# Kernel optimization log

Measured on AMD Instinct MI355X. Metric: run time of the kernel, lower is better.

## Reference

```python
import jax, jax.numpy as jnp
import numpy as np

TAU = 5.0
ENTROPY_REG = 0.0  # entropy branch disabled (matches init kwargs)
NEG_INF = -1.0e9
NORM_EPS = 1e-12   # F.normalize eps
COS_EPS = 1e-8     # F.cosine_similarity eps


def _l2norm(x):
    n = jnp.sqrt(jnp.sum(x * x, axis=-1, keepdims=True))
    return x / jnp.maximum(n, NORM_EPS)


def setup_inputs() -> dict:
    key = jax.random.key(0)
    k1, k2, k3 = jax.random.split(key, 3)
    B, T, D = 8, 2048, 512
    pred_tokens = jax.random.normal(k1, (B, T, D), dtype=jnp.float32)
    text_tokens = jax.random.normal(k2, (B, T, D), dtype=jnp.float32)
    text_pad_mask = jax.random.randint(k3, (B, T), 0, 2).astype(jnp.bool_)  # True = PAD
    return {"pred_tokens": pred_tokens, "text_tokens": text_tokens, "text_pad_mask": text_pad_mask}


def reference(pred_tokens, text_tokens, text_pad_mask):
    B, Tp, D = pred_tokens.shape
    Tt = text_tokens.shape[1]
    T = min(Tp, Tt)
    P = _l2norm(pred_tokens[:, :T, :])            # [B,T,D]
    E = _l2norm(text_tokens[:, :T, :])            # [B,T,D]
    valid = ~text_pad_mask[:, :T]                 # [B,T] True = valid column

    S = jnp.einsum('btd,bsd->bts', P, E)          # [B,T,T]
    S = jnp.where(valid[:, None, :], S, NEG_INF)
    A = jax.nn.softmax(S * TAU, axis=-1)          # [B,T,T]
    E_hat = jnp.einsum('bts,bsd->btd', A, E)      # [B,T,D]

    # cosine similarity with eps-clamped norms (F.cosine_similarity semantics)
    dot = jnp.sum(P * E_hat, axis=-1)             # [B,T]
    pn = jnp.maximum(jnp.sqrt(jnp.sum(P * P, axis=-1)), COS_EPS)
    en = jnp.maximum(jnp.sqrt(jnp.sum(E_hat * E_hat, axis=-1)), COS_EPS)
    cos = dot / (pn * en)                         # [B,T]

    # row_has_valid: per-batch 'any valid column', broadcast over rows
    row_valid = jnp.broadcast_to(jnp.any(valid, axis=-1, keepdims=True), cos.shape)
    w = row_valid.astype(cos.dtype)
    cnt = jnp.sum(w)
    loss_sel = jnp.sum(w * (1.0 - cos)) / jnp.maximum(cnt, 1.0)
    loss = jnp.where(cnt > 0, loss_sel, jnp.zeros((), cos.dtype))
    tas = jnp.where(cnt > 0, 1.0 - jax.lax.stop_gradient(loss), loss)
    return (loss, tas)
```

## Files before the change

kernel.cpp:

```cpp
#include <hip/hip_runtime.h>
#include <cstdint>

typedef float f32x4 __attribute__((ext_vector_type(4)));
typedef long longx2 __attribute__((ext_vector_type(2)));
typedef unsigned char u8;
typedef unsigned short u16;
typedef unsigned int u32;
typedef unsigned long long u64;

#define B_N 8
#define T_N 2048
#define D_N 512
#define TAU 5.0f
#define NROW (B_N * T_N)
#define K1E 7.213475204444817f
#define K2E 1.4426950408889634f

#define WAITV(n) asm volatile("s_waitcnt vmcnt(" #n ")" ::: "memory")
#define BAR      __builtin_amdgcn_s_barrier()

__device__ __forceinline__ void gload_lds16(const u8* g, u8* l) {
  __builtin_amdgcn_global_load_lds(
      (const __attribute__((address_space(1))) u32*)g,
      (__attribute__((address_space(3))) u32*)l, 16, 0, 0);
}

__device__ __forceinline__ u32 pk4_fp8(float a, float b, float c, float d) {
  int w = __builtin_amdgcn_cvt_pk_fp8_f32(a, b, 0, 0);
  w = __builtin_amdgcn_cvt_pk_fp8_f32(c, d, w, 1);
  return (u32)w;
}

__device__ __forceinline__ u16 f2bf16(float x) {
  u32 u = __builtin_bit_cast(u32, x);
  u32 r = u + 0x7fffu + ((u >> 16) & 1u);
  return (u16)(r >> 16);
}
__device__ __forceinline__ float bf2f(u16 v) {
  u32 u = ((u32)v) << 16;
  return __builtin_bit_cast(float, u);
}

__global__ void kprep(const float* __restrict__ text,
                      u8* __restrict__ EF, u8* __restrict__ ET) {
  __shared__ u8 tile[32][528];
  int b = blockIdx.y, t = blockIdx.x;
  int tr = threadIdx.x;
  int row = tr >> 3, seg = tr & 7;
  const float* src = text + ((size_t)b * T_N + t * 32 + row) * D_N + seg * 64;
  float4 v[16];
  float ss = 0.f;
#pragma unroll
  for (int j = 0; j < 16; ++j) {
    v[j] = *(const float4*)(src + j * 4);
    ss += v[j].x*v[j].x + v[j].y*v[j].y + v[j].z*v[j].z + v[j].w*v[j].w;
  }
  ss += __shfl_xor(ss, 1); ss += __shfl_xor(ss, 2); ss += __shfl_xor(ss, 4);
  float inv = 1.f / fmaxf(sqrtf(ss), 1e-12f);
  u32 w[16];
#pragma unroll
  for (int j = 0; j < 16; ++j)
    w[j] = pk4_fp8(v[j].x*inv, v[j].y*inv, v[j].z*inv, v[j].w*inv);
  uint4* ldst = (uint4*)&tile[row][seg * 64];
#pragma unroll
  for (int j = 0; j < 4; ++j)
    ldst[j] = make_uint4(w[4*j], w[4*j+1], w[4*j+2], w[4*j+3]);
  __syncthreads();
  size_t tbase = ((size_t)(b * 64 + t)) << 14;
  {
    int j = tr >> 5, tok = tr & 31;
    u32 acc[16];
#pragma unroll
    for (int g2 = 0; g2 < 4; ++g2)
#pragma unroll
      for (int h = 0; h < 2; ++h) {
        uint2 vv = *(const uint2*)&tile[tok][j*64 + h*32 + g2*8];
        acc[g2*4 + h*2] = vv.x; acc[g2*4 + h*2 + 1] = vv.y;
      }
    uint4* dst = (uint4*)(EF + tbase + tr * 64);
#pragma unroll
    for (int q = 0; q < 4; ++q)
      dst[q] = make_uint4(acc[4*q], acc[4*q+1], acc[4*q+2], acc[4*q+3]);
  }
  {
    int m = tr >> 4, g2 = (tr >> 2) & 3, c0 = (tr & 3) * 4;
    u32 acc[16];
#pragma unroll
    for (int ci = 0; ci < 4; ++ci)
#pragma unroll
      for (int h = 0; h < 2; ++h) {
        int c = c0 + ci, n = 2*m + h;
        u32 lo = 0, hi = 0;
#pragma unroll
        for (int e = 0; e < 4; ++e) lo |= (u32)tile[g2*4 + e][n*16 + c] << (8*e);
#pragma unroll
        for (int e = 0; e < 4; ++e) hi |= (u32)tile[16 + g2*4 + e][n*16 + c] << (8*e);
        acc[ci*4 + h*2] = lo; acc[ci*4 + h*2 + 1] = hi;
      }
    uint4* dst = (uint4*)(ET + tbase + tr * 64);
#pragma unroll
    for (int q = 0; q < 4; ++q)
      dst[q] = make_uint4(acc[4*q], acc[4*q+1], acc[4*q+2], acc[4*q+3]);
  }
}

__launch_bounds__(512, 2)
__global__ void kflash(const float* __restrict__ pred,
                       const u8* __restrict__ EF, const u8* __restrict__ ET,
                       const int* __restrict__ mask,
                       u16* __restrict__ Opart, float* __restrict__ Lpart,
                       float* __restrict__ Dpart) {
  int b = blockIdx.x & 7;
  int rem = blockIdx.x >> 3;
  int rb = rem & 15, h = rem >> 4;
  int wid = threadIdx.x >> 6, lane = threadIdx.x & 63;
  int g = lane >> 4, c = lane & 15;
  int row0 = rb * 128 + wid * 16;
  int t0 = h * 32;

  __shared__ u64 mbits[32];
  __shared__ __align__(16) u8 els[2][16384];
  __shared__ __align__(16) u8 etls[2][16384];

  const u8* EFb = EF + (((size_t)(b * 64)) << 14) + (lane << 4);
  const u8* ETb = ET + (((size_t)(b * 64)) << 14) + (lane << 4);

  auto stageE = [&](int buf, int t) {
    size_t tb = ((size_t)t) << 14;
#pragma unroll
    for (int j = 0; j < 2; ++j) {
      int ch = wid * 2 + j;
      gload_lds16(EFb + tb + (ch << 10), &els[buf][ch << 10]);
    }
  };
  auto stageET = [&](int buf, int t) {
    size_t tb = ((size_t)t) << 14;
#pragma unroll
    for (int j = 0; j < 2; ++j) {
      int ch = wid * 2 + j;
      gload_lds16(ETb + tb + (ch << 10), &etls[buf][ch << 10]);
    }
  };

  for (int chunk = wid; chunk < 32; chunk += 8) {
    int col = chunk * 64 + lane;
    u64 bal = __ballot(mask[b * T_N + col] == 0);
    if (lane == 0) mbits[chunk] = bal;
  }

  stageE(0, t0); stageET(0, t0); stageE(1, t0 + 1);

  long pf[16];
  {
    int prow = row0 + c;
    const float* pr = pred + ((size_t)(b * T_N) + prow) * D_N;
    float ss = 0.f;
#pragma unroll
    for (int kk = 0; kk < 16; ++kk) {
      float4 v0 = *(const float4*)(pr + kk * 32 + g * 8);
      float4 v1 = *(const float4*)(pr + kk * 32 + g * 8 + 4);
      ss += v0.x*v0.x + v0.y*v0.y + v0.z*v0.z + v0.w*v0.w
          + v1.x*v1.x + v1.y*v1.y + v1.z*v1.z + v1.w*v1.w;
    }
    ss += __shfl_xor(ss, 16);
    ss += __shfl_xor(ss, 32);
    float inv = 1.f / fmaxf(sqrtf(ss), 1e-12f);
#pragma unroll
    for (int kk = 0; kk < 16; ++kk) {
      float4 v0 = *(const float4*)(pr + kk * 32 + g * 8);
      float4 v1 = *(const float4*)(pr + kk * 32 + g * 8 + 4);
      u32 lo = pk4_fp8(v0.x*inv, v0.y*inv, v0.z*inv, v0.w*inv);
      u32 hi = pk4_fp8(v1.x*inv, v1.y*inv, v1.z*inv, v1.w*inv);
      pf[kk] = (long)(((u64)hi << 32) | lo);
    }
  }

  __syncthreads();

  f32x4 zero = {0.f, 0.f, 0.f, 0.f};
  f32x4 eh[32];
#pragma unroll
  for (int n = 0; n < 32; ++n) eh[n] = zero;
  float lsum = 0.f, dsum = 0.f;

  const int sb_off = c * 64 + g * 16;
  const int pv_off = g * 256 + c * 16;

#pragma unroll 1
  for (int tt = 0; tt < 32; ++tt) {
    int cur = tt & 1;
    if (tt < 31) { WAITV(2); } else { WAITV(0); }
    BAR;

    if (tt < 31) stageET(cur ^ 1, t0 + tt + 1);
    const u8* el = &els[cur][0];
    f32x4 ta0 = zero, tb0 = zero, ta1 = zero, tb1 = zero;
    __builtin_amdgcn_s_setprio(1);
#pragma unroll
    for (int j = 0; j < 4; ++j) {
      longx2 b0 = *(const longx2*)(el + j * 2048 + sb_off);
      longx2 b1 = *(const longx2*)(el + j * 2048 + 1024 + sb_off);
      ta0 = __builtin_amdgcn_mfma_f32_16x16x32_fp8_fp8(b0[0], pf[2*j],   ta0, 0, 0, 0);
      tb0 = __builtin_amdgcn_mfma_f32_16x16x32_fp8_fp8(b0[1], pf[2*j+1], tb0, 0, 0, 0);
      ta1 = __builtin_amdgcn_mfma_f32_16x16x32_fp8_fp8(b1[0], pf[2*j],   ta1, 0, 0, 0);
      tb1 = __builtin_amdgcn_mfma_f32_16x16x32_fp8_fp8(b1[1], pf[2*j+1], tb1, 0, 0, 0);
    }
    __builtin_amdgcn_s_setprio(0);
    BAR;

    __builtin_amdgcn_s_setprio(1);
#pragma unroll
    for (int j = 4; j < 8; ++j) {
      longx2 b0 = *(const longx2*)(el + j * 2048 + sb_off);
      longx2 b1 = *(const longx2*)(el + j * 2048 + 1024 + sb_off);
      ta0 = __builtin_amdgcn_mfma_f32_16x16x32_fp8_fp8(b0[0], pf[2*j],   ta0, 0, 0, 0);
      tb0 = __builtin_amdgcn_mfma_f32_16x16x32_fp8_fp8(b0[1], pf[2*j+1], tb0, 0, 0, 0);
      ta1 = __builtin_amdgcn_mfma_f32_16x16x32_fp8_fp8(b1[0], pf[2*j],   ta1, 0, 0, 0);
      tb1 = __builtin_amdgcn_mfma_f32_16x16x32_fp8_fp8(b1[1], pf[2*j+1], tb1, 0, 0, 0);
    }
    __builtin_amdgcn_s_setprio(0);
    f32x4 st0 = ta0 + tb0, st1 = ta1 + tb1;
    BAR;

    if (tt < 30) stageE(cur, t0 + tt + 2);
    int c0 = (t0 + tt) * 32;
    u64 mw = mbits[c0 >> 6];
    u32 sh0 = (c0 & 63) + g * 4;
    u32 bits0 = (u32)(mw >> sh0) & 0xf;
    u32 bits1 = (u32)(mw >> (sh0 + 16)) & 0xf;
    float p0[4], p1[4];
#pragma unroll
    for (int r = 0; r < 4; ++r) {
      p0[r] = (bits0 >> r) & 1 ? __builtin_exp2f(fmaf(K1E, st0[r], -K2E)) : 0.f;
      p1[r] = (bits1 >> r) & 1 ? __builtin_exp2f(fmaf(K1E, st1[r], -K2E)) : 0.f;
      lsum += p0[r] + p1[r];
      dsum += p0[r] * st0[r] + p1[r] * st1[r];
    }
    u32 lo = pk4_fp8(p0[0], p0[1], p0[2], p0[3]);
    u32 hi = pk4_fp8(p1[0], p1[1], p1[2], p1[3]);
    long af = (long)(((u64)hi << 32) | lo);

    const u8* et = &etls[cur][0];
    __builtin_amdgcn_s_setprio(1);
#pragma unroll
    for (int m = 0; m < 8; ++m) {
      longx2 bv = *(const longx2*)(et + m * 1024 + pv_off);
      eh[2*m]   = __builtin_amdgcn_mfma_f32_16x16x32_fp8_fp8(af, bv[0], eh[2*m],   0, 0, 0);
      eh[2*m+1] = __builtin_amdgcn_mfma_f32_16x16x32_fp8_fp8(af, bv[1], eh[2*m+1], 0, 0, 0);
    }
    __builtin_amdgcn_s_setprio(0);
    BAR;

    __builtin_amdgcn_s_setprio(1);
#pragma unroll
    for (int m = 8; m < 16; ++m) {
      longx2 bv = *(const longx2*)(et + m * 1024 + pv_off);
      eh[2*m]   = __builtin_amdgcn_mfma_f32_16x16x32_fp8_fp8(af, bv[0], eh[2*m],   0, 0, 0);
      eh[2*m+1] = __builtin_amdgcn_mfma_f32_16x16x32_fp8_fp8(af, bv[1], eh[2*m+1], 0, 0, 0);
    }
    __builtin_amdgcn_s_setprio(0);
  }

  lsum += __shfl_xor(lsum, 16);
  lsum += __shfl_xor(lsum, 32);
  dsum += __shfl_xor(dsum, 16);
  dsum += __shfl_xor(dsum, 32);
  u16* OP = Opart + (size_t)h * ((size_t)NROW * D_N);
#pragma unroll
  for (int r = 0; r < 4; ++r) {
    int brow = b * T_N + row0 + g * 4 + r;
    u16* orow = OP + (size_t)brow * D_N + c;
#pragma unroll
    for (int n = 0; n < 32; ++n) orow[n * 16] = f2bf16(eh[n][r]);
  }
  if (g == 0) {
    Lpart[h * NROW + b * T_N + row0 + c] = lsum;
    Dpart[h * NROW + b * T_N + row0 + c] = dsum;
  }
}

__global__ void kcomb(const u16* __restrict__ Opart, const float* __restrict__ Lpart,
                      const float* __restrict__ Dpart,
                      float* __restrict__ pl, float* __restrict__ pw) {
  __shared__ float sl[8], swv[8];
  int tr = threadIdx.x;
  int row = blockIdx.x * 8 + (tr >> 5);
  int ln = tr & 31;
  float l = Lpart[row] + Lpart[NROW + row];
  float dot = Dpart[row] + Dpart[NROW + row];
  const u16* o0 = Opart + (size_t)row * D_N + ln * 16;
  const u16* o1 = o0 + (size_t)NROW * D_N;
  float e2 = 0.f;
#pragma unroll
  for (int q = 0; q < 2; ++q) {
    uint4 a0 = *(const uint4*)(o0 + q * 8);
    uint4 a1 = *(const uint4*)(o1 + q * 8);
    u32 w0[4] = {a0.x, a0.y, a0.z, a0.w};
    u32 w1[4] = {a1.x, a1.y, a1.z, a1.w};
#pragma unroll
    for (int j = 0; j < 8; ++j) {
      float f0 = bf2f((u16)((w0[j >> 1] >> ((j & 1) * 16)) & 0xffff));
      float f1 = bf2f((u16)((w1[j >> 1] >> ((j & 1) * 16)) & 0xffff));
      float ev = f0 + f1;
      e2 += ev * ev;
    }
  }
#pragma unroll
  for (int msk = 16; msk >= 1; msk >>= 1) e2 += __shfl_xor(e2, msk);
  if (ln == 0) {
    float w = (l > 0.f) ? 1.f : 0.f;
    float cosv = (l > 0.f) ? dot / fmaxf(sqrtf(e2), 1e-8f * l) : 0.f;
    sl[tr >> 5] = w * (1.f - cosv);
    swv[tr >> 5] = w;
  }
  __syncthreads();
  if (tr == 0) {
    float a = 0.f, b2 = 0.f;
#pragma unroll
    for (int i = 0; i < 8; ++i) { a += sl[i]; b2 += swv[i]; }
    pl[blockIdx.x] = a;
    pw[blockIdx.x] = b2;
  }
}

__global__ void kreduce(const float* __restrict__ pl, const float* __restrict__ pw,
                        float* __restrict__ out) {
  __shared__ float sm[256], sw[256];
  float s = 0.f, w = 0.f;
  for (int i = threadIdx.x; i < NROW / 8; i += 256) { s += pl[i]; w += pw[i]; }
  sm[threadIdx.x] = s; sw[threadIdx.x] = w;
  __syncthreads();
#pragma unroll
  for (int st = 128; st >= 1; st >>= 1) {
    if ((int)threadIdx.x < st) {
      sm[threadIdx.x] += sm[threadIdx.x + st];
      sw[threadIdx.x] += sw[threadIdx.x + st];
    }
    __syncthreads();
  }
  if (threadIdx.x == 0) {
    float cnt = sw[0];
    float loss = (cnt > 0.f) ? sm[0] / fmaxf(cnt, 1.f) : 0.f;
    out[0] = loss;
    out[1] = (cnt > 0.f) ? 1.f - loss : 0.f;
  }
}

extern "C" void kernel_launch(void* const* d_in, const int* in_sizes, int n_in,
                              void* d_out, int out_size, void* d_ws, size_t ws_size,
                              hipStream_t stream) {
  const float* pred = (const float*)d_in[0];
  const float* text = (const float*)d_in[1];
  const int* mask = (const int*)d_in[2];
  char* ws = (char*)d_ws;
  const size_t EB8 = (size_t)B_N * T_N * D_N;
  const size_t OB = (size_t)NROW * D_N * 2;
  u8* EF = (u8*)ws;
  u8* ET = (u8*)(ws + EB8);
  u16* Opart = (u16*)(ws + 2 * EB8);
  char* base2 = ws + 2 * EB8 + 2 * OB;
  float* Lpart = (float*)(base2);
  float* Dpart = (float*)(base2 + 131072);
  float* pl = (float*)(base2 + 262144);
  float* pw = (float*)(base2 + 262144 + 16384);
  float* out = (float*)d_out;

  kprep<<<dim3(64, 8), dim3(256), 0, stream>>>(text, EF, ET);
  kflash<<<dim3(256), dim3(512), 0, stream>>>(pred, EF, ET, mask, Opart, Lpart, Dpart);
  kcomb<<<dim3(NROW / 8), dim3(256), 0, stream>>>(Opart, Lpart, Dpart, pl, pw);
  kreduce<<<dim3(1), dim3(256), 0, stream>>>(pl, pw, out);
}
```

Measured before the change: 103.5 us.

## Repartition flash kernel waves: split columns for QK and D-dimension for PV via LDS

Each wave now computes scores for two 16-row query groups over a 16-column half of the key tile, writes fp8 probabilities to a new shared buffer, and then does the PV product over all 128 rows but only its own 64-wide slice of D. Each wave therefore loads only two ET fragments per step instead of sixteen, and the per-wave accumulator set becomes 8x4 tiles. The ET transpose layout is changed to match the new fragment order. The goal is less LDS read traffic and fewer barriers per step, at the cost of an extra LDS write/read round trip for P, an lgkmcnt wait, and cross-wave reduction of the row sums through shared memory.

```diff
diff --git a/kernel.cpp b/kernel.cpp
--- a/kernel.cpp
+++ b/kernel.cpp
@@ -17,6 +17,7 @@
 #define K2E 1.4426950408889634f
 
 #define WAITV(n) asm volatile("s_waitcnt vmcnt(" #n ")" ::: "memory")
+#define WAITL0   asm volatile("s_waitcnt lgkmcnt(0)" ::: "memory")
 #define BAR      __builtin_amdgcn_s_barrier()
 
 __device__ __forceinline__ void gload_lds16(const u8* g, u8* l) {
@@ -92,9 +93,9 @@
         int c = c0 + ci, n = 2*m + h;
         u32 lo = 0, hi = 0;
 #pragma unroll
-        for (int e = 0; e < 4; ++e) lo |= (u32)tile[g2*4 + e][n*16 + c] << (8*e);
-#pragma unroll
-        for (int e = 0; e < 4; ++e) hi |= (u32)tile[16 + g2*4 + e][n*16 + c] << (8*e);
+        for (int e = 0; e < 4; ++e) lo |= (u32)tile[g2*8 + e][n*16 + c] << (8*e);
+#pragma unroll
+        for (int e = 0; e < 4; ++e) hi |= (u32)tile[g2*8 + 4 + e][n*16 + c] << (8*e);
         acc[ci*4 + h*2] = lo; acc[ci*4 + h*2 + 1] = hi;
       }
     uint4* dst = (uint4*)(ET + tbase + tr * 64);
@@ -115,12 +116,15 @@
   int rb = rem & 15, h = rem >> 4;
   int wid = threadIdx.x >> 6, lane = threadIdx.x & 63;
   int g = lane >> 4, c = lane & 15;
-  int row0 = rb * 128 + wid * 16;
+  int rq = wid >> 1, hw = wid & 1;
+  int Q0 = rq * 2;
   int t0 = h * 32;
 
   __shared__ u64 mbits[32];
   __shared__ __align__(16) u8 els[2][16384];
   __shared__ __align__(16) u8 etls[2][16384];
+  __shared__ __align__(16) u8 plds[2][6144];
+  __shared__ float Lbuf[2][128], Dbuf[2][128];
 
   const u8* EFb = EF + (((size_t)(b * 64)) << 14) + (lane << 4);
   const u8* ETb = ET + (((size_t)(b * 64)) << 14) + (lane << 4);
@@ -150,9 +154,10 @@
 
   stageE(0, t0); stageET(0, t0); stageE(1, t0 + 1);
 
-  long pf[16];
-  {
-    int prow = row0 + c;
+  long pf2[2][16];
+#pragma unroll
+  for (int q = 0; q < 2; ++q) {
+    int prow = rb * 128 + (Q0 + q) * 16 + c;
     const float* pr = pred + ((size_t)(b * T_N) + prow) * D_N;
     float ss = 0.f;
 #pragma unroll
@@ -171,20 +176,24 @@
       float4 v1 = *(const float4*)(pr + kk * 32 + g * 8 + 4);
       u32 lo = pk4_fp8(v0.x*inv, v0.y*inv, v0.z*inv, v0.w*inv);
       u32 hi = pk4_fp8(v1.x*inv, v1.y*inv, v1.z*inv, v1.w*inv);
-      pf[kk] = (long)(((u64)hi << 32) | lo);
+      pf2[q][kk] = (long)(((u64)hi << 32) | lo);
     }
   }
 
   __syncthreads();
 
   f32x4 zero = {0.f, 0.f, 0.f, 0.f};
-  f32x4 eh[32];
-#pragma unroll
-  for (int n = 0; n < 32; ++n) eh[n] = zero;
-  float lsum = 0.f, dsum = 0.f;
-
-  const int sb_off = c * 64 + g * 16;
-  const int pv_off = g * 256 + c * 16;
+  f32x4 eh[8][4];
+#pragma unroll
+  for (int q = 0; q < 8; ++q)
+#pragma unroll
+    for (int n = 0; n < 4; ++n) eh[q][n] = zero;
+  float lsum[2] = {0.f, 0.f}, dsum[2] = {0.f, 0.f};
+
+  const int sA_off = (hw * 16 + c) * 64 + g * 16;
+  const int pvB_off = g * 256 + c * 16;
+  const int pA_off = c * 48 + g * 8;
+  const int pW_off = c * 48 + hw * 16 + g * 4;
 
 #pragma unroll 1
   for (int tt = 0; tt < 32; ++tt) {
@@ -194,88 +203,82 @@
 
     if (tt < 31) stageET(cur ^ 1, t0 + tt + 1);
     const u8* el = &els[cur][0];
-    f32x4 ta0 = zero, tb0 = zero, ta1 = zero, tb1 = zero;
+    f32x4 a00 = zero, a01 = zero, a10 = zero, a11 = zero;
     __builtin_amdgcn_s_setprio(1);
 #pragma unroll
-    for (int j = 0; j < 4; ++j) {
-      longx2 b0 = *(const longx2*)(el + j * 2048 + sb_off);
-      longx2 b1 = *(const longx2*)(el + j * 2048 + 1024 + sb_off);
-      ta0 = __builtin_amdgcn_mfma_f32_16x16x32_fp8_fp8(b0[0], pf[2*j],   ta0, 0, 0, 0);
-      tb0 = __builtin_amdgcn_mfma_f32_16x16x32_fp8_fp8(b0[1], pf[2*j+1], tb0, 0, 0, 0);
-      ta1 = __builtin_amdgcn_mfma_f32_16x16x32_fp8_fp8(b1[0], pf[2*j],   ta1, 0, 0, 0);
-      tb1 = __builtin_amdgcn_mfma_f32_16x16x32_fp8_fp8(b1[1], pf[2*j+1], tb1, 0, 0, 0);
+    for (int j = 0; j < 8; ++j) {
+      longx2 av = *(const longx2*)(el + j * 2048 + sA_off);
+      a00 = __builtin_amdgcn_mfma_f32_16x16x32_fp8_fp8(av[0], pf2[0][2*j],   a00, 0, 0, 0);
+      a01 = __builtin_amdgcn_mfma_f32_16x16x32_fp8_fp8(av[1], pf2[0][2*j+1], a01, 0, 0, 0);
+      a10 = __builtin_amdgcn_mfma_f32_16x16x32_fp8_fp8(av[0], pf2[1][2*j],   a10, 0, 0, 0);
+      a11 = __builtin_amdgcn_mfma_f32_16x16x32_fp8_fp8(av[1], pf2[1][2*j+1], a11, 0, 0, 0);
     }
     __builtin_amdgcn_s_setprio(0);
+    f32x4 st0 = a00 + a01, st1 = a10 + a11;
+
+    int cb = (t0 + tt) * 32;
+    u64 mw = mbits[cb >> 6];
+    u32 sh = (u32)(cb & 63) + hw * 16 + g * 4;
+    u32 bits = (u32)(mw >> sh) & 0xf;
+    float p0[4], p1[4];
+#pragma unroll
+    for (int r = 0; r < 4; ++r) {
+      p0[r] = (bits >> r) & 1 ? __builtin_exp2f(fmaf(K1E, st0[r], -K2E)) : 0.f;
+      p1[r] = (bits >> r) & 1 ? __builtin_exp2f(fmaf(K1E, st1[r], -K2E)) : 0.f;
+      lsum[0] += p0[r]; dsum[0] += p0[r] * st0[r];
+      lsum[1] += p1[r]; dsum[1] += p1[r] * st1[r];
+    }
+    *(u32*)(&plds[cur][Q0 * 768 + pW_off])       = pk4_fp8(p0[0], p0[1], p0[2], p0[3]);
+    *(u32*)(&plds[cur][(Q0 + 1) * 768 + pW_off]) = pk4_fp8(p1[0], p1[1], p1[2], p1[3]);
+    WAITL0;
     BAR;
 
+    if (tt < 30) stageE(cur, t0 + tt + 2);
+    const u8* et = &etls[cur][0];
+    const u8* pl = &plds[cur][0];
+    longx2 bv0 = *(const longx2*)(et + (wid * 2) * 1024 + pvB_off);
+    longx2 bv1 = *(const longx2*)(et + (wid * 2 + 1) * 1024 + pvB_off);
     __builtin_amdgcn_s_setprio(1);
 #pragma unroll
-    for (int j = 4; j < 8; ++j) {
-      longx2 b0 = *(const longx2*)(el + j * 2048 + sb_off);
-      longx2 b1 = *(const longx2*)(el + j * 2048 + 1024 + sb_off);
-      ta0 = __builtin_amdgcn_mfma_f32_16x16x32_fp8_fp8(b0[0], pf[2*j],   ta0, 0, 0, 0);
-      tb0 = __builtin_amdgcn_mfma_f32_16x16x32_fp8_fp8(b0[1], pf[2*j+1], tb0, 0, 0, 0);
-      ta1 = __builtin_amdgcn_mfma_f32_16x16x32_fp8_fp8(b1[0], pf[2*j],   ta1, 0, 0, 0);
-      tb1 = __builtin_amdgcn_mfma_f32_16x16x32_fp8_fp8(b1[1], pf[2*j+1], tb1, 0, 0, 0);
+    for (int q = 0; q < 8; ++q) {
+      long af = *(const long*)(pl + q * 768 + pA_off);
+      eh[q][0] = __builtin_amdgcn_mfma_f32_16x16x32_fp8_fp8(af, bv0[0], eh[q][0], 0, 0, 0);
+      eh[q][1] = __builtin_amdgcn_mfma_f32_16x16x32_fp8_fp8(af, bv0[1], eh[q][1], 0, 0, 0);
+      eh[q][2] = __builtin_amdgcn_mfma_f32_16x16x32_fp8_fp8(af, bv1[0], eh[q][2], 0, 0, 0);
+      eh[q][3] = __builtin_amdgcn_mfma_f32_16x16x32_fp8_fp8(af, bv1[1], eh[q][3], 0, 0, 0);
     }
     __builtin_amdgcn_s_setprio(0);
-    f32x4 st0 = ta0 + tb0, st1 = ta1 + tb1;
-    BAR;
-
-    if (tt < 30) stageE(cur, t0 + tt + 2);
-    int c0 = (t0 + tt) * 32;
-    u64 mw = mbits[c0 >> 6];
-    u32 sh0 = (c0 & 63) + g * 4;
-    u32 bits0 = (u32)(mw >> sh0) & 0xf;
-    u32 bits1 = (u32)(mw >> (sh0 + 16)) & 0xf;
-    float p0[4], p1[4];
-#pragma unroll
-    for (int r = 0; r < 4; ++r) {
-      p0[r] = (bits0 >> r) & 1 ? __builtin_exp2f(fmaf(K1E, st0[r], -K2E)) : 0.f;
-      p1[r] = (bits1 >> r) & 1 ? __builtin_exp2f(fmaf(K1E, st1[r], -K2E)) : 0.f;
-      lsum += p0[r] + p1[r];
-      dsum += p0[r] * st0[r] + p1[r] * st1[r];
-    }
-    u32 lo = pk4_fp8(p0[0], p0[1], p0[2], p0[3]);
-    u32 hi = pk4_fp8(p1[0], p1[1], p1[2], p1[3]);
-    long af = (long)(((u64)hi << 32) | lo);
-
-    const u8* et = &etls[cur][0];
-    __builtin_amdgcn_s_setprio(1);
-#pragma unroll
-    for (int m = 0; m < 8; ++m) {
-      longx2 bv = *(const longx2*)(et + m * 1024 + pv_off);
-      eh[2*m]   = __builtin_amdgcn_mfma_f32_16x16x32_fp8_fp8(af, bv[0], eh[2*m],   0, 0, 0);
-      eh[2*m+1] = __builtin_amdgcn_mfma_f32_16x16x32_fp8_fp8(af, bv[1], eh[2*m+1], 0, 0, 0);
-    }
-    __builtin_amdgcn_s_setprio(0);
-    BAR;
-
-    __builtin_amdgcn_s_setprio(1);
-#pragma unroll
-    for (int m = 8; m < 16; ++m) {
-      longx2 bv = *(const longx2*)(et + m * 1024 + pv_off);
-      eh[2*m]   = __builtin_amdgcn_mfma_f32_16x16x32_fp8_fp8(af, bv[0], eh[2*m],   0, 0, 0);
-      eh[2*m+1] = __builtin_amdgcn_mfma_f32_16x16x32_fp8_fp8(af, bv[1], eh[2*m+1], 0, 0, 0);
-    }
-    __builtin_amdgcn_s_setprio(0);
-  }
-
-  lsum += __shfl_xor(lsum, 16);
-  lsum += __shfl_xor(lsum, 32);
-  dsum += __shfl_xor(dsum, 16);
-  dsum += __shfl_xor(dsum, 32);
+  }
+
+#pragma unroll
+  for (int q = 0; q < 2; ++q) {
+    lsum[q] += __shfl_xor(lsum[q], 16); lsum[q] += __shfl_xor(lsum[q], 32);
+    dsum[q] += __shfl_xor(dsum[q], 16); dsum[q] += __shfl_xor(dsum[q], 32);
+  }
+  if (g == 0) {
+#pragma unroll
+    for (int q = 0; q < 2; ++q) {
+      Lbuf[hw][(Q0 + q) * 16 + c] = lsum[q];
+      Dbuf[hw][(Q0 + q) * 16 + c] = dsum[q];
+    }
+  }
+
   u16* OP = Opart + (size_t)h * ((size_t)NROW * D_N);
-#pragma unroll
-  for (int r = 0; r < 4; ++r) {
-    int brow = b * T_N + row0 + g * 4 + r;
-    u16* orow = OP + (size_t)brow * D_N + c;
-#pragma unroll
-    for (int n = 0; n < 32; ++n) orow[n * 16] = f2bf16(eh[n][r]);
-  }
-  if (g == 0) {
-    Lpart[h * NROW + b * T_N + row0 + c] = lsum;
-    Dpart[h * NROW + b * T_N + row0 + c] = dsum;
+  int bT = b * T_N + rb * 128;
+#pragma unroll
+  for (int q = 0; q < 8; ++q)
+#pragma unroll
+    for (int n = 0; n < 4; ++n) {
+      int brow = bT + q * 16 + 4 * g;
+      u16* orow = OP + (size_t)brow * D_N + wid * 64 + n * 16 + c;
+#pragma unroll
+      for (int r = 0; r < 4; ++r) orow[(size_t)r * D_N] = f2bf16(eh[q][n][r]);
+    }
+  __syncthreads();
+  if (threadIdx.x < 128) {
+    int row = threadIdx.x;
+    Lpart[h * NROW + bT + row] = Lbuf[0][row] + Lbuf[1][row];
+    Dpart[h * NROW + bT + row] = Dbuf[0][row] + Dbuf[1][row];
   }
 }
 
```

New measurement: 115.1 us. 1.11x slower.

## Relayout EF tiles for lane-contiguous LDS reads, prefetch fragments, drop mid-phase barriers

Applied to the files above, without the earlier changes.

The prep kernel now writes the normalized fp8 E tiles in an order where each lane's MFMA operand sits at lane*16, so LDS reads in the flash kernel become contiguous 16-byte per-lane accesses. The QK and PV loops are merged into single loops that double-buffer their LDS fragment loads in registers, prefetching the next fragment before issuing the current MFMAs. The intra-phase barriers that split each loop in half are removed, which cuts synchronization but lets waves drift further apart within an iteration. It also raises register pressure from the extra fragment buffers.

```diff
diff --git a/kernel.cpp b/kernel.cpp
--- a/kernel.cpp
+++ b/kernel.cpp
@@ -69,18 +69,13 @@
   size_t tbase = ((size_t)(b * 64 + t)) << 14;
   {
     int j = tr >> 5, tok = tr & 31;
-    u32 acc[16];
-#pragma unroll
-    for (int g2 = 0; g2 < 4; ++g2)
-#pragma unroll
-      for (int h = 0; h < 2; ++h) {
-        uint2 vv = *(const uint2*)&tile[tok][j*64 + h*32 + g2*8];
-        acc[g2*4 + h*2] = vv.x; acc[g2*4 + h*2 + 1] = vv.y;
-      }
-    uint4* dst = (uint4*)(EF + tbase + tr * 64);
-#pragma unroll
-    for (int q = 0; q < 4; ++q)
-      dst[q] = make_uint4(acc[4*q], acc[4*q+1], acc[4*q+2], acc[4*q+3]);
+    u8* base = EF + tbase + j * 2048 + ((tok >> 4) << 10) + ((tok & 15) << 4);
+#pragma unroll
+    for (int g2 = 0; g2 < 4; ++g2) {
+      uint2 h0 = *(const uint2*)&tile[tok][j*64 + g2*8];
+      uint2 h1 = *(const uint2*)&tile[tok][j*64 + 32 + g2*8];
+      *(uint4*)(base + g2 * 256) = make_uint4(h0.x, h0.y, h1.x, h1.y);
+    }
   }
   {
     int m = tr >> 4, g2 = (tr >> 2) & 3, c0 = (tr & 3) * 4;
@@ -117,13 +112,14 @@
   int g = lane >> 4, c = lane & 15;
   int row0 = rb * 128 + wid * 16;
   int t0 = h * 32;
+  const int l16 = lane << 4;
 
   __shared__ u64 mbits[32];
   __shared__ __align__(16) u8 els[2][16384];
   __shared__ __align__(16) u8 etls[2][16384];
 
-  const u8* EFb = EF + (((size_t)(b * 64)) << 14) + (lane << 4);
-  const u8* ETb = ET + (((size_t)(b * 64)) << 14) + (lane << 4);
+  const u8* EFb = EF + (((size_t)(b * 64)) << 14) + l16;
+  const u8* ETb = ET + (((size_t)(b * 64)) << 14) + l16;
 
   auto stageE = [&](int buf, int t) {
     size_t tb = ((size_t)t) << 14;
@@ -183,9 +179,6 @@
   for (int n = 0; n < 32; ++n) eh[n] = zero;
   float lsum = 0.f, dsum = 0.f;
 
-  const int sb_off = c * 64 + g * 16;
-  const int pv_off = g * 256 + c * 16;
-
 #pragma unroll 1
   for (int tt = 0; tt < 32; ++tt) {
     int cur = tt & 1;
@@ -194,32 +187,25 @@
 
     if (tt < 31) stageET(cur ^ 1, t0 + tt + 1);
     const u8* el = &els[cur][0];
-    f32x4 ta0 = zero, tb0 = zero, ta1 = zero, tb1 = zero;
+    longx2 rS0[2], rS1[2];
+    rS0[0] = *(const longx2*)(el + l16);
+    rS1[0] = *(const longx2*)(el + 1024 + l16);
+    f32x4 a00 = zero, a01 = zero, a10 = zero, a11 = zero;
     __builtin_amdgcn_s_setprio(1);
 #pragma unroll
-    for (int j = 0; j < 4; ++j) {
-      longx2 b0 = *(const longx2*)(el + j * 2048 + sb_off);
-      longx2 b1 = *(const longx2*)(el + j * 2048 + 1024 + sb_off);
-      ta0 = __builtin_amdgcn_mfma_f32_16x16x32_fp8_fp8(b0[0], pf[2*j],   ta0, 0, 0, 0);
-      tb0 = __builtin_amdgcn_mfma_f32_16x16x32_fp8_fp8(b0[1], pf[2*j+1], tb0, 0, 0, 0);
-      ta1 = __builtin_amdgcn_mfma_f32_16x16x32_fp8_fp8(b1[0], pf[2*j],   ta1, 0, 0, 0);
-      tb1 = __builtin_amdgcn_mfma_f32_16x16x32_fp8_fp8(b1[1], pf[2*j+1], tb1, 0, 0, 0);
+    for (int j = 0; j < 8; ++j) {
+      int pp = j & 1;
+      if (j < 7) {
+        rS0[pp ^ 1] = *(const longx2*)(el + (j + 1) * 2048 + l16);
+        rS1[pp ^ 1] = *(const longx2*)(el + (j + 1) * 2048 + 1024 + l16);
+      }
+      a00 = __builtin_amdgcn_mfma_f32_16x16x32_fp8_fp8(rS0[pp][0], pf[2*j],   a00, 0, 0, 0);
+      a01 = __builtin_amdgcn_mfma_f32_16x16x32_fp8_fp8(rS0[pp][1], pf[2*j+1], a01, 0, 0, 0);
+      a10 = __builtin_amdgcn_mfma_f32_16x16x32_fp8_fp8(rS1[pp][0], pf[2*j],   a10, 0, 0, 0);
+      a11 = __builtin_amdgcn_mfma_f32_16x16x32_fp8_fp8(rS1[pp][1], pf[2*j+1], a11, 0, 0, 0);
     }
     __builtin_amdgcn_s_setprio(0);
-    BAR;
-
-    __builtin_amdgcn_s_setprio(1);
-#pragma unroll
-    for (int j = 4; j < 8; ++j) {
-      longx2 b0 = *(const longx2*)(el + j * 2048 + sb_off);
-      longx2 b1 = *(const longx2*)(el + j * 2048 + 1024 + sb_off);
-      ta0 = __builtin_amdgcn_mfma_f32_16x16x32_fp8_fp8(b0[0], pf[2*j],   ta0, 0, 0, 0);
-      tb0 = __builtin_amdgcn_mfma_f32_16x16x32_fp8_fp8(b0[1], pf[2*j+1], tb0, 0, 0, 0);
-      ta1 = __builtin_amdgcn_mfma_f32_16x16x32_fp8_fp8(b1[0], pf[2*j],   ta1, 0, 0, 0);
-      tb1 = __builtin_amdgcn_mfma_f32_16x16x32_fp8_fp8(b1[1], pf[2*j+1], tb1, 0, 0, 0);
-    }
-    __builtin_amdgcn_s_setprio(0);
-    f32x4 st0 = ta0 + tb0, st1 = ta1 + tb1;
+    f32x4 st0 = a00 + a01, st1 = a10 + a11;
     BAR;
 
     if (tt < 30) stageE(cur, t0 + tt + 2);
@@ -241,22 +227,15 @@
     long af = (long)(((u64)hi << 32) | lo);
 
     const u8* et = &etls[cur][0];
+    longx2 rV[2];
+    rV[0] = *(const longx2*)(et + l16);
     __builtin_amdgcn_s_setprio(1);
 #pragma unroll
-    for (int m = 0; m < 8; ++m) {
-      longx2 bv = *(const longx2*)(et + m * 1024 + pv_off);
-      eh[2*m]   = __builtin_amdgcn_mfma_f32_16x16x32_fp8_fp8(af, bv[0], eh[2*m],   0, 0, 0);
-      eh[2*m+1] = __builtin_amdgcn_mfma_f32_16x16x32_fp8_fp8(af, bv[1], eh[2*m+1], 0, 0, 0);
-    }
-    __builtin_amdgcn_s_setprio(0);
-    BAR;
-
-    __builtin_amdgcn_s_setprio(1);
-#pragma unroll
-    for (int m = 8; m < 16; ++m) {
-      longx2 bv = *(const longx2*)(et + m * 1024 + pv_off);
-      eh[2*m]   = __builtin_amdgcn_mfma_f32_16x16x32_fp8_fp8(af, bv[0], eh[2*m],   0, 0, 0);
-      eh[2*m+1] = __builtin_amdgcn_mfma_f32_16x16x32_fp8_fp8(af, bv[1], eh[2*m+1], 0, 0, 0);
+    for (int m = 0; m < 16; ++m) {
+      int pp = m & 1;
+      if (m < 15) rV[pp ^ 1] = *(const longx2*)(et + (m + 1) * 1024 + l16);
+      eh[2*m]   = __builtin_amdgcn_mfma_f32_16x16x32_fp8_fp8(af, rV[pp][0], eh[2*m],   0, 0, 0);
+      eh[2*m+1] = __builtin_amdgcn_mfma_f32_16x16x32_fp8_fp8(af, rV[pp][1], eh[2*m+1], 0, 0, 0);
     }
     __builtin_amdgcn_s_setprio(0);
   }
```

Result: no change. 105.0 us (+1.5%).
